# Kernel tuning notes

Measured on AMD Instinct MI355X. Metric: run time of the kernel, lower is better.

## Reference

```python
import jax, jax.numpy as jnp
import numpy as np

D_MODEL = 1024
NUM_HEADS = 16
HEAD_DIM = D_MODEL // NUM_HEADS
SCALE = HEAD_DIM ** -0.5
LN_EPS = 1e-5
Q_EPS = 1e-5


def bit_quant(W):
    # BitNet b1.58 ternary weight quantization with straight-through estimator.
    gamma = jnp.mean(jnp.abs(W))
    Wq = jnp.clip(jnp.round(W / (gamma + Q_EPS)), -1.0, 1.0) * gamma
    return W + jax.lax.stop_gradient(Wq - W)


def layer_norm(x, gamma, beta):
    mu = jnp.mean(x, axis=-1, keepdims=True)
    var = jnp.mean(jnp.square(x - mu), axis=-1, keepdims=True)
    return (x - mu) * jax.lax.rsqrt(var + LN_EPS) * gamma + beta


def setup_inputs() -> dict:
    key = jax.random.key(0)
    ks = jax.random.split(key, 8)
    B, T, T_ctx, C = 4, 1024, 2048, D_MODEL
    w_std = C ** -0.5
    return {
        "x": jax.random.normal(ks[0], (B, T, C), jnp.float32),
        "context": jax.random.normal(ks[1], (B, T_ctx, C), jnp.float32),
        "Wq": jax.random.normal(ks[2], (C, C), jnp.float32) * w_std,
        "bq": jnp.zeros((C,), jnp.float32),
        "Wk": jax.random.normal(ks[3], (C, C), jnp.float32) * w_std,
        "bk": jnp.zeros((C,), jnp.float32),
        "Wv": jax.random.normal(ks[4], (C, C), jnp.float32) * w_std,
        "bv": jnp.zeros((C,), jnp.float32),
        "Wo": jax.random.normal(ks[5], (C, C), jnp.float32) * w_std,
        "bo": jnp.zeros((C,), jnp.float32),
        "ln_gamma": jnp.ones((C,), jnp.float32),
        "ln_beta": jnp.zeros((C,), jnp.float32),
    }


def reference(x, context, Wq, bq, Wk, bk, Wv, bv, Wo, bo, ln_gamma, ln_beta):
    B, T, C = x.shape
    T_ctx = context.shape[1]
    residual = x
    xn = layer_norm(x, ln_gamma, ln_beta)
    # BitNet-quantized projections (torch Linear: y = x @ W.T + b)
    q = xn @ bit_quant(Wq).T + bq                      # [B,T,C]
    k = context @ bit_quant(Wk).T + bk                 # [B,T_ctx,C]
    v = context @ bit_quant(Wv).T + bv                 # [B,T_ctx,C]
    q = q.reshape(B, T, NUM_HEADS, HEAD_DIM)
    k = k.reshape(B, T_ctx, NUM_HEADS, HEAD_DIM)
    v = v.reshape(B, T_ctx, NUM_HEADS, HEAD_DIM)
    scores = jnp.einsum("bqhd,bkhd->bhqk", q, k) * SCALE   # [B,H,T,T_ctx]
    probs = jax.nn.softmax(scores, axis=-1)
    out = jnp.einsum("bhqk,bkhd->bqhd", probs, v).reshape(B, T, C)
    return residual + (out @ bit_quant(Wo).T + bo)
```

## Files before the change

kernel.cpp:

```cpp
#include <hip/hip_runtime.h>
#include <hip/hip_bf16.h>

typedef __attribute__((ext_vector_type(8))) short s8x;
typedef __attribute__((ext_vector_type(4))) float f4x;
typedef unsigned short u16;
typedef unsigned int u32;

#define T_ 1024
#define TC_ 2048
#define SCLOG2E 0.1803368801111243f

#define WAIT_VM(n) asm volatile("s_waitcnt vmcnt(" #n ")" ::: "memory")

__device__ __forceinline__ u16 f2bf(float f) {
    u32 u = __float_as_uint(f);
    return (u16)((u + 0x7fffu + ((u >> 16) & 1u)) >> 16);
}

#if defined(__has_builtin)
#if __has_builtin(__builtin_amdgcn_cvt_pk_bf16_f32)
#define HAVE_PK 1
#endif
#endif

__device__ __forceinline__ u32 pack2bf(float a, float b) {
#ifdef HAVE_PK
    typedef __attribute__((ext_vector_type(2))) __bf16 bf2t;
    bf2t r = __builtin_amdgcn_cvt_pk_bf16_f32(a, b);
    u32 u;
    __builtin_memcpy(&u, &r, 4);
    return u;
#else
    return (u32)f2bf(a) | ((u32)f2bf(b) << 16);
#endif
}

__device__ __forceinline__ void gload16(const void* g, void* l) {
    __builtin_amdgcn_global_load_lds((const __attribute__((address_space(1))) u32*)g,
                                     (__attribute__((address_space(3))) u32*)l, 16, 0, 0);
}

__global__ __launch_bounds__(256) void absmean_k(const float* __restrict__ W0, const float* __restrict__ W1,
                                                 const float* __restrict__ W2, const float* __restrict__ W3,
                                                 float* __restrict__ gsum) {
    int wi = blockIdx.y;
    const float* W = (wi == 0) ? W0 : (wi == 1) ? W1 : (wi == 2) ? W2 : W3;
    const int n4 = (1024 * 1024) / 4;
    float s = 0.f;
    int stride = gridDim.x * blockDim.x;
    for (int i = blockIdx.x * blockDim.x + threadIdx.x; i < n4; i += stride) {
        float4 v = ((const float4*)W)[i];
        s += fabsf(v.x) + fabsf(v.y) + fabsf(v.z) + fabsf(v.w);
    }
#pragma unroll
    for (int off = 32; off; off >>= 1) s += __shfl_down(s, off, 64);
    __shared__ float ps[4];
    if ((threadIdx.x & 63) == 0) ps[threadIdx.x >> 6] = s;
    __syncthreads();
    if (threadIdx.x == 0) atomicAdd(gsum + wi, ps[0] + ps[1] + ps[2] + ps[3]);
}

__global__ __launch_bounds__(256) void prep_k(
        const float* __restrict__ x, const float* __restrict__ lng, const float* __restrict__ lnb,
        u16* __restrict__ xn,
        const float* __restrict__ ctx, u16* __restrict__ ctxb,
        const float* __restrict__ W0, const float* __restrict__ W1,
        const float* __restrict__ W2, const float* __restrict__ W3,
        u16* __restrict__ D0, u16* __restrict__ D1, u16* __restrict__ D2, u16* __restrict__ D3,
        const float* __restrict__ gsum) {
    __shared__ float ps[8];
    int bx = blockIdx.x, t = threadIdx.x;
    if (bx < 4096) {
        int row = bx;
        float4 xv = ((const float4*)(x + (long)row * 1024))[t];
        float s = xv.x + xv.y + xv.z + xv.w;
        float s2 = xv.x * xv.x + xv.y * xv.y + xv.z * xv.z + xv.w * xv.w;
#pragma unroll
        for (int off = 32; off; off >>= 1) { s += __shfl_down(s, off, 64); s2 += __shfl_down(s2, off, 64); }
        if ((t & 63) == 0) { ps[t >> 6] = s; ps[4 + (t >> 6)] = s2; }
        __syncthreads();
        float S = ps[0] + ps[1] + ps[2] + ps[3];
        float S2 = ps[4] + ps[5] + ps[6] + ps[7];
        float mu = S * (1.f / 1024.f);
        float var = S2 * (1.f / 1024.f) - mu * mu;
        float rstd = rsqrtf(var + 1e-5f);
        float4 gv = ((const float4*)lng)[t];
        float4 bv = ((const float4*)lnb)[t];
        uint2 o;
        o.x = pack2bf((xv.x - mu) * rstd * gv.x + bv.x, (xv.y - mu) * rstd * gv.y + bv.y);
        o.y = pack2bf((xv.z - mu) * rstd * gv.z + bv.z, (xv.w - mu) * rstd * gv.w + bv.w);
        ((uint2*)(xn + (long)row * 1024))[t] = o;
    } else if (bx < 12288) {
        int i = (bx - 4096) * 256 + t;
        float4 v = ((const float4*)ctx)[i];
        uint2 o = {pack2bf(v.x, v.y), pack2bf(v.z, v.w)};
        ((uint2*)ctxb)[i] = o;
    } else {
        int wi = (bx - 12288) >> 10;
        const float* W = (wi == 0) ? W0 : (wi == 1) ? W1 : (wi == 2) ? W2 : W3;
        u16* D = (wi == 0) ? D0 : (wi == 1) ? D1 : (wi == 2) ? D2 : D3;
        float inv = 1.0f / (gsum[wi] * (1.0f / 1048576.0f) + 1e-5f);
        int i = ((bx - 12288) & 1023) * 256 + t;
        float4 wv = ((const float4*)W)[i];
        uint2 o;
        o.x = pack2bf(fminf(1.f, fmaxf(-1.f, rintf(wv.x * inv))),
                      fminf(1.f, fmaxf(-1.f, rintf(wv.y * inv))));
        o.y = pack2bf(fminf(1.f, fmaxf(-1.f, rintf(wv.z * inv))),
                      fminf(1.f, fmaxf(-1.f, rintf(wv.w * inv))));
        ((uint2*)D)[i] = o;
    }
}

__global__ __launch_bounds__(256) void gemm_fused(
        const u16* __restrict__ xn, const u16* __restrict__ ctxb,
        const u16* __restrict__ wtq, const u16* __restrict__ wtk, const u16* __restrict__ wtv,
        const float* __restrict__ bq, const float* __restrict__ bk, const float* __restrict__ bv,
        const float* __restrict__ gsum,
        u16* __restrict__ qb, u16* __restrict__ kb, u16* __restrict__ vtb) {
    __shared__ __align__(16) char smem[49152];
    int tid = threadIdx.x;
    int w = tid >> 6, l = tid & 63, lq = l & 15, lh = l >> 4;
    int wm = (w >> 1) * 64, wn = (w & 1) * 64;
    int bx = blockIdx.x;
    int xcd = bx & 7;
    int prob, m0, n0, gidx;
    const u16 *A, *Wt;
    const float* bias;
    float sc;
    if (bx < 256) {
        int local = bx >> 3;
        prob = 0; A = xn; Wt = wtq; bias = bq; sc = SCLOG2E; gidx = 0;
        m0 = (xcd * 4 + (local & 3)) * 128;
        n0 = (local >> 2) * 128;
    } else {
        int b = bx - 256;
        int local3 = b >> 3;
        int kv = local3 & 1;
        int idx = local3 >> 1;
        prob = 1 + kv; A = ctxb;
        Wt = kv ? wtv : wtk; bias = kv ? bv : bk; sc = 1.0f; gidx = 1 + kv;
        m0 = (xcd * 8 + (idx & 7)) * 128;
        n0 = (idx >> 3) * 128;
    }
    int sp = tid >> 3, ss = tid & 7;
    int st = ss ^ (sp & 7);
    int r0 = sp * 2 + (st >> 2), c0 = st & 3;
    const u16* Ag0 = A + (long)(m0 + r0) * 1024 + c0 * 8;
    const u16* Ag1 = Ag0 + 64 * 1024;
    const u16* Bg0 = Wt + (long)(n0 + r0) * 1024 + c0 * 8;
    const u16* Bg1 = Bg0 + 64 * 1024;
    int aoff[4], boff[4];
#pragma unroll
    for (int i = 0; i < 4; i++) {
        int ar = wm + i * 16 + lq, ap = ar >> 1;
        aoff[i] = ap * 128 + (((((ar & 1) << 2) | lh) ^ (ap & 7)) * 16);
        int br = wn + i * 16 + lq, bp = br >> 1;
        boff[i] = bp * 128 + (((((br & 1) << 2) | lh) ^ (bp & 7)) * 16);
    }
    f4x acc[4][4] = {};
#define STAGE_G(kt, buf)                                                   \
    {                                                                      \
        char* Ad = smem + (buf) * 16384;                                   \
        char* Bd = Ad + 8192;                                              \
        gload16(Ag0 + (kt) * 32, Ad + tid * 16);                           \
        gload16(Ag1 + (kt) * 32, Ad + 4096 + tid * 16);                    \
        gload16(Bg0 + (kt) * 32, Bd + tid * 16);                           \
        gload16(Bg1 + (kt) * 32, Bd + 4096 + tid * 16);                    \
    }
    STAGE_G(0, 0);
    STAGE_G(1, 1);
#pragma unroll
    for (int kt = 0; kt < 32; kt++) {
        if (kt < 31) { WAIT_VM(4); } else { WAIT_VM(0); }
        __builtin_amdgcn_s_barrier();
        if (kt + 2 < 32) STAGE_G(kt + 2, (kt + 2) % 3);
        const char* Ac = smem + (kt % 3) * 16384;
        const char* Bc = Ac + 8192;
        s8x af[4], bfr[4];
#pragma unroll
        for (int i = 0; i < 4; i++) {
            af[i] = *(const s8x*)(Ac + aoff[i]);
            bfr[i] = *(const s8x*)(Bc + boff[i]);
        }
#pragma unroll
        for (int i = 0; i < 4; i++)
#pragma unroll
            for (int j = 0; j < 4; j++)
                acc[i][j] = __builtin_amdgcn_mfma_f32_16x16x32_bf16(af[i], bfr[j], acc[i][j], 0, 0, 0);
    }
    float gamma = gsum[gidx] * (1.0f / 1048576.0f) * sc;
    if (prob < 2) {
        u16* outq = (prob == 0) ? qb : kb;
        int tshift = (prob == 0) ? 10 : 11;
        int tmask = (1 << tshift) - 1;
#pragma unroll
        for (int i = 0; i < 4; i++) {
            int gr = m0 + wm + i * 16 + lh * 4;
#pragma unroll
            for (int j = 0; j < 4; j++) {
                int gc = n0 + wn + j * 16 + lq;
                float bb = bias[gc] * sc;
                int h = gc >> 6, d = gc & 63;
#pragma unroll
                for (int r = 0; r < 4; r++) {
                    int row = gr + r;
                    int bidx = row >> tshift, tt = row & tmask;
                    outq[((((long)(bidx * 16 + h)) << tshift) + tt) * 64 + d] = f2bf(acc[i][j][r] * gamma + bb);
                }
            }
        }
    } else {
        __syncthreads();
        char* Ct = smem;
#pragma unroll
        for (int i = 0; i < 4; i++) {
            int tt = wm + i * 16 + lh * 4;
#pragma unroll
            for (int j = 0; j < 4; j++) {
                int c = wn + j * 16 + lq;
                float bb = bias[n0 + c];
                uint2 pk;
                pk.x = pack2bf(acc[i][j][0] * gamma + bb, acc[i][j][1] * gamma + bb);
                pk.y = pack2bf(acc[i][j][2] * gamma + bb, acc[i][j][3] * gamma + bb);
                int slot = (tt >> 3) ^ (c & 15);
                *(uint2*)(Ct + c * 256 + slot * 16 + (tt & 7) * 2) = pk;
            }
        }
        __syncthreads();
        int bb2 = m0 >> 11, t0 = m0 & 2047;
#pragma unroll
        for (int it = 0; it < 8; it++) {
            int e = it * 256 + tid;
            int c = e >> 4, ch = e & 15;
            int slot = ch ^ (c & 15);
            s8x v = *(const s8x*)(Ct + c * 256 + slot * 16);
            int gcg = n0 + c;
            int h = gcg >> 6, d = gcg & 63;
            *(s8x*)(vtb + ((long)((bb2 * 16 + h) * 64 + d)) * TC_ + t0 + ch * 8) = v;
        }
    }
}

__global__ __launch_bounds__(256) void gemm_o(const u16* __restrict__ A, const u16* __restrict__ Wt,
                                              const float* __restrict__ bias, const float* __restrict__ gsum,
                                              const float* __restrict__ residual, float* __restrict__ outr) {
    __shared__ __align__(16) char smem[36864];
    int tid = threadIdx.x;
    int w = tid >> 6, l = tid & 63, lq = l & 15, lh = l >> 4;
    int wm = (w >> 1) * 64, wn = (w & 1) * 32;
    int bx = blockIdx.x;
    int xcd = bx & 7, local = bx >> 3;
    int m0 = (xcd * 4 + (local & 3)) * 128;
    int n0 = (local >> 2) * 64;
    int sp = tid >> 3, ss = tid & 7;
    int st = ss ^ (sp & 7);
    int r0 = sp * 2 + (st >> 2), c0 = st & 3;
    const u16* Ag0 = A + (long)(m0 + r0) * 1024 + c0 * 8;
    const u16* Ag1 = Ag0 + 64 * 1024;
    const u16* Bg0 = Wt + (long)(n0 + r0) * 1024 + c0 * 8;
    int aoff[4], boff[2];
#pragma unroll
    for (int i = 0; i < 4; i++) {
        int ar = wm + i * 16 + lq, ap = ar >> 1;
        aoff[i] = ap * 128 + (((((ar & 1) << 2) | lh) ^ (ap & 7)) * 16);
    }
#pragma unroll
    for (int j = 0; j < 2; j++) {
        int br = wn + j * 16 + lq, bp = br >> 1;
        boff[j] = bp * 128 + (((((br & 1) << 2) | lh) ^ (bp & 7)) * 16);
    }
    f4x acc[4][2] = {};
#define STAGE_O(kt, buf)                                                   \
    {                                                                      \
        char* Ad = smem + (buf) * 12288;                                   \
        char* Bd = Ad + 8192;                                              \
        gload16(Ag0 + (kt) * 32, Ad + tid * 16);                           \
        gload16(Ag1 + (kt) * 32, Ad + 4096 + tid * 16);                    \
        gload16(Bg0 + (kt) * 32, Bd + tid * 16);                           \
    }
    STAGE_O(0, 0);
    STAGE_O(1, 1);
#pragma unroll
    for (int kt = 0; kt < 32; kt++) {
        if (kt < 31) { WAIT_VM(3); } else { WAIT_VM(0); }
        __builtin_amdgcn_s_barrier();
        if (kt + 2 < 32) STAGE_O(kt + 2, (kt + 2) % 3);
        const char* Ac = smem + (kt % 3) * 12288;
        const char* Bc = Ac + 8192;
        s8x af[4], bfr[2];
#pragma unroll
        for (int i = 0; i < 4; i++) af[i] = *(const s8x*)(Ac + aoff[i]);
#pragma unroll
        for (int j = 0; j < 2; j++) bfr[j] = *(const s8x*)(Bc + boff[j]);
#pragma unroll
        for (int i = 0; i < 4; i++)
#pragma unroll
            for (int j = 0; j < 2; j++)
                acc[i][j] = __builtin_amdgcn_mfma_f32_16x16x32_bf16(af[i], bfr[j], acc[i][j], 0, 0, 0);
    }
    float gamma = gsum[3] * (1.0f / 1048576.0f);
#pragma unroll
    for (int i = 0; i < 4; i++) {
        int gr = m0 + wm + i * 16 + lh * 4;
#pragma unroll
        for (int j = 0; j < 2; j++) {
            int gc = n0 + wn + j * 16 + lq;
            float bb = bias[gc];
#pragma unroll
            for (int r = 0; r < 4; r++) {
                long idx = (long)(gr + r) * 1024 + gc;
                outr[idx] = residual[idx] + acc[i][j][r] * gamma + bb;
            }
        }
    }
}

__global__ __launch_bounds__(256) void attn_k(const u16* __restrict__ qh, const u16* __restrict__ kh,
                                              const u16* __restrict__ vth, u16* __restrict__ attn) {
    __shared__ __align__(16) char smem[51200];
    int tid = threadIdx.x, w = tid >> 6, l = tid & 63, lq = l & 15, lh = l >> 4;
    int bh = blockIdx.x, q0 = blockIdx.y * 128;
    const u16* qp = qh + ((long)bh * T_ + q0) * 64;
    const u16* kp = kh + (long)bh * TC_ * 64;
    const u16* vp = vth + (long)bh * 64 * TC_;
#pragma unroll
    for (int i = 0; i < 4; i++) {
        int cid = i * 256 + tid;
        int r = cid >> 3, c = (cid & 7) ^ (r & 7);
        gload16(qp + r * 64 + c * 8, smem + cid * 16);
    }
    __syncthreads();
    s8x qf[2][2];
#pragma unroll
    for (int nb = 0; nb < 2; nb++)
#pragma unroll
        for (int dh = 0; dh < 2; dh++) {
            int qrow = w * 32 + nb * 16 + lq;
            int ch = (dh * 4 + lh) ^ (qrow & 7);
            qf[nb][dh] = *(const s8x*)(smem + qrow * 128 + ch * 16);
        }
    __syncthreads();
#define STAGE_KV(kt, buf)                                                          \
    {                                                                              \
        char* Kb = smem + (buf) * 16384;                                           \
        char* Vb = Kb + 8192;                                                      \
        _Pragma("unroll") for (int i = 0; i < 2; i++) {                            \
            int cid = i * 256 + tid;                                               \
            int r = cid >> 3, c = (cid & 7) ^ (r & 7);                             \
            gload16(kp + ((kt) * 64 + r) * 64 + c * 8, Kb + cid * 16);             \
            gload16(vp + (long)r * TC_ + (kt) * 64 + c * 8, Vb + cid * 16);        \
        }                                                                          \
    }
    STAGE_KV(0, 0);
    f4x oacc[2][4] = {};
    f4x lrun[2] = {};
    const s8x ones = {16256, 16256, 16256, 16256, 16256, 16256, 16256, 16256};
    char* Psb = smem + 32768 + w * 4608;
    for (int kt = 0; kt < TC_ / 64; kt++) {
        __syncthreads();
        if (kt + 1 < TC_ / 64) STAGE_KV(kt + 1, (kt + 1) & 1);
        char* Ksb = smem + (kt & 1) * 16384;
        char* Vsb = Ksb + 8192;
        f4x z[2][4];
#pragma unroll
        for (int ni = 0; ni < 4; ni++) {
            int kr = ni * 16 + lq;
            s8x a0 = *(const s8x*)(Ksb + kr * 128 + ((lh) ^ (kr & 7)) * 16);
            s8x a1 = *(const s8x*)(Ksb + kr * 128 + ((4 + lh) ^ (kr & 7)) * 16);
#pragma unroll
            for (int nb = 0; nb < 2; nb++) {
                f4x zz = {0.f, 0.f, 0.f, 0.f};
                zz = __builtin_amdgcn_mfma_f32_16x16x32_bf16(a0, qf[nb][0], zz, 0, 0, 0);
                zz = __builtin_amdgcn_mfma_f32_16x16x32_bf16(a1, qf[nb][1], zz, 0, 0, 0);
                z[nb][ni] = zz;
            }
        }
#pragma unroll
        for (int nb = 0; nb < 2; nb++) {
            int prow = nb * 16 + lq;
#pragma unroll
            for (int ni = 0; ni < 4; ni++) {
                uint2 pk;
                pk.x = pack2bf(__builtin_amdgcn_exp2f(z[nb][ni][0]), __builtin_amdgcn_exp2f(z[nb][ni][1]));
                pk.y = pack2bf(__builtin_amdgcn_exp2f(z[nb][ni][2]), __builtin_amdgcn_exp2f(z[nb][ni][3]));
                *(uint2*)(Psb + prow * 144 + ni * 32 + lh * 8) = pk;
            }
        }
        s8x vf[4][2];
#pragma unroll
        for (int nd = 0; nd < 4; nd++) {
            int vr = nd * 16 + lq;
            vf[nd][0] = *(const s8x*)(Vsb + vr * 128 + ((lh) ^ (vr & 7)) * 16);
            vf[nd][1] = *(const s8x*)(Vsb + vr * 128 + ((4 + lh) ^ (vr & 7)) * 16);
        }
#pragma unroll
        for (int qb = 0; qb < 2; qb++) {
            int prow = qb * 16 + lq;
            s8x pf0 = *(const s8x*)(Psb + prow * 144 + lh * 16);
            s8x pf1 = *(const s8x*)(Psb + prow * 144 + 64 + lh * 16);
            f4x rs = {0.f, 0.f, 0.f, 0.f};
            rs = __builtin_amdgcn_mfma_f32_16x16x32_bf16(pf0, ones, rs, 0, 0, 0);
            rs = __builtin_amdgcn_mfma_f32_16x16x32_bf16(pf1, ones, rs, 0, 0, 0);
#pragma unroll
            for (int r = 0; r < 4; r++) lrun[qb][r] += rs[r];
#pragma unroll
            for (int nd = 0; nd < 4; nd++) {
                oacc[qb][nd] = __builtin_amdgcn_mfma_f32_16x16x32_bf16(pf0, vf[nd][0], oacc[qb][nd], 0, 0, 0);
                oacc[qb][nd] = __builtin_amdgcn_mfma_f32_16x16x32_bf16(pf1, vf[nd][1], oacc[qb][nd], 0, 0, 0);
            }
        }
    }
    int b = bh >> 4, h = bh & 15;
#pragma unroll
    for (int qb = 0; qb < 2; qb++)
#pragma unroll
        for (int r = 0; r < 4; r++) {
            int q = q0 + w * 32 + qb * 16 + lh * 4 + r;
            float rcp = 1.f / lrun[qb][r];
#pragma unroll
            for (int nd = 0; nd < 4; nd++)
                attn[((long)(b * T_ + q)) * 1024 + h * 64 + nd * 16 + lq] = f2bf(oacc[qb][nd][r] * rcp);
        }
}

extern "C" void kernel_launch(void* const* d_in, const int* in_sizes, int n_in,
                              void* d_out, int out_size, void* d_ws, size_t ws_size,
                              hipStream_t stream) {
    const float* x   = (const float*)d_in[0];
    const float* ctx = (const float*)d_in[1];
    const float* Wq  = (const float*)d_in[2];
    const float* bq  = (const float*)d_in[3];
    const float* Wk  = (const float*)d_in[4];
    const float* bk  = (const float*)d_in[5];
    const float* Wv  = (const float*)d_in[6];
    const float* bv  = (const float*)d_in[7];
    const float* Wo  = (const float*)d_in[8];
    const float* bo  = (const float*)d_in[9];
    const float* lng = (const float*)d_in[10];
    const float* lnb = (const float*)d_in[11];
    float* out = (float*)d_out;

    char* ws = (char*)d_ws;
    float* gsum = (float*)ws;
    size_t off = 256;
    u16* wtq  = (u16*)(ws + off); off += (size_t)1024 * 1024 * 2;
    u16* wtk  = (u16*)(ws + off); off += (size_t)1024 * 1024 * 2;
    u16* wtv  = (u16*)(ws + off); off += (size_t)1024 * 1024 * 2;
    u16* wto  = (u16*)(ws + off); off += (size_t)1024 * 1024 * 2;
    u16* ctxb = (u16*)(ws + off); off += (size_t)8192 * 1024 * 2;
    u16* xn   = (u16*)(ws + off); off += (size_t)4096 * 1024 * 2;
    u16* qb_  = (u16*)(ws + off); off += (size_t)4096 * 1024 * 2;
    u16* kb   = (u16*)(ws + off); off += (size_t)8192 * 1024 * 2;
    u16* vtb  = (u16*)(ws + off); off += (size_t)8192 * 1024 * 2;
    u16* attnb = xn;

    hipMemsetAsync(gsum, 0, 16, stream);
    absmean_k<<<dim3(128, 4), 256, 0, stream>>>(Wq, Wk, Wv, Wo, gsum);
    prep_k<<<16384, 256, 0, stream>>>(x, lng, lnb, xn, ctx, ctxb,
                                      Wq, Wk, Wv, Wo, wtq, wtk, wtv, wto, gsum);
    gemm_fused<<<1280, 256, 0, stream>>>(xn, ctxb, wtq, wtk, wtv, bq, bk, bv, gsum, qb_, kb, vtb);
    attn_k<<<dim3(64, 8), 256, 0, stream>>>(qb_, kb, vtb, attnb);
    gemm_o<<<512, 256, 0, stream>>>(attnb, wto, bo, gsum, x, out);
}
```

Baseline: 254.1 us.

## Keep attention probabilities in registers and triple-buffer K/V loads

The attention kernel now computes S^T tiles and feeds the exponentiated probabilities directly from registers into 16x16x16 bf16 MFMAs that produce the transposed output. This removes the LDS round-trip for P and the extra ones-MFMA used for row sums, which are now accumulated in VALU and reduced with cross-lane shuffles at the end. K/V staging moves from double to triple buffering with explicit vmcnt waits and raw barriers, and the loop is fully unrolled. In exchange it uses more MFMA instructions of a smaller shape and puts more pressure on registers and on the unrolled code size.

```diff
diff --git a/kernel.cpp b/kernel.cpp
--- a/kernel.cpp
+++ b/kernel.cpp
@@ -2,6 +2,7 @@
 #include <hip/hip_bf16.h>
 
 typedef __attribute__((ext_vector_type(8))) short s8x;
+typedef __attribute__((ext_vector_type(4))) short s4x;
 typedef __attribute__((ext_vector_type(4))) float f4x;
 typedef unsigned short u16;
 typedef unsigned int u32;
@@ -20,6 +21,9 @@
 #if defined(__has_builtin)
 #if __has_builtin(__builtin_amdgcn_cvt_pk_bf16_f32)
 #define HAVE_PK 1
+#endif
+#if __has_builtin(__builtin_amdgcn_mfma_f32_16x16x16bf16_1k)
+#define HAVE_MFMA16 1
 #endif
 #endif
 
@@ -32,6 +36,16 @@
     return u;
 #else
     return (u32)f2bf(a) | ((u32)f2bf(b) << 16);
+#endif
+}
+
+__device__ __forceinline__ f4x mfma16(s4x a, s4x b, f4x c) {
+#ifdef HAVE_MFMA16
+    return __builtin_amdgcn_mfma_f32_16x16x16bf16_1k(a, b, c, 0, 0, 0);
+#else
+    f4x d = c;
+    asm volatile("v_mfma_f32_16x16x16_bf16 %0, %1, %2, %0" : "+v"(d) : "v"(a), "v"(b));
+    return d;
 #endif
 }
 
@@ -317,7 +331,7 @@
 
 __global__ __launch_bounds__(256) void attn_k(const u16* __restrict__ qh, const u16* __restrict__ kh,
                                               const u16* __restrict__ vth, u16* __restrict__ attn) {
-    __shared__ __align__(16) char smem[51200];
+    __shared__ __align__(16) char smem[49152];
     int tid = threadIdx.x, w = tid >> 6, l = tid & 63, lq = l & 15, lh = l >> 4;
     int bh = blockIdx.x, q0 = blockIdx.y * 128;
     const u16* qp = qh + ((long)bh * T_ + q0) * 64;
@@ -327,7 +341,7 @@
     for (int i = 0; i < 4; i++) {
         int cid = i * 256 + tid;
         int r = cid >> 3, c = (cid & 7) ^ (r & 7);
-        gload16(qp + r * 64 + c * 8, smem + cid * 16);
+        gload16(qp + r * 64 + c * 8, smem + 32768 + cid * 16);
     }
     __syncthreads();
     s8x qf[2][2];
@@ -337,90 +351,91 @@
         for (int dh = 0; dh < 2; dh++) {
             int qrow = w * 32 + nb * 16 + lq;
             int ch = (dh * 4 + lh) ^ (qrow & 7);
-            qf[nb][dh] = *(const s8x*)(smem + qrow * 128 + ch * 16);
+            qf[nb][dh] = *(const s8x*)(smem + 32768 + qrow * 128 + ch * 16);
         }
     __syncthreads();
 #define STAGE_KV(kt, buf)                                                          \
     {                                                                              \
         char* Kb = smem + (buf) * 16384;                                           \
         char* Vb = Kb + 8192;                                                      \
-        _Pragma("unroll") for (int i = 0; i < 2; i++) {                            \
-            int cid = i * 256 + tid;                                               \
-            int r = cid >> 3, c = (cid & 7) ^ (r & 7);                             \
-            gload16(kp + ((kt) * 64 + r) * 64 + c * 8, Kb + cid * 16);             \
-            gload16(vp + (long)r * TC_ + (kt) * 64 + c * 8, Vb + cid * 16);        \
-        }                                                                          \
+        int r = tid >> 3, c = (tid & 7) ^ (r & 7);                                 \
+        gload16(kp + ((kt) * 64 + r) * 64 + c * 8, Kb + tid * 16);                 \
+        gload16(kp + ((kt) * 64 + r + 32) * 64 + c * 8, Kb + 4096 + tid * 16);     \
+        gload16(vp + (long)r * TC_ + (kt) * 64 + c * 8, Vb + tid * 16);            \
+        gload16(vp + (long)(r + 32) * TC_ + (kt) * 64 + c * 8, Vb + 4096 + tid * 16); \
     }
     STAGE_KV(0, 0);
-    f4x oacc[2][4] = {};
-    f4x lrun[2] = {};
-    const s8x ones = {16256, 16256, 16256, 16256, 16256, 16256, 16256, 16256};
-    char* Psb = smem + 32768 + w * 4608;
-    for (int kt = 0; kt < TC_ / 64; kt++) {
-        __syncthreads();
-        if (kt + 1 < TC_ / 64) STAGE_KV(kt + 1, (kt + 1) & 1);
-        char* Ksb = smem + (kt & 1) * 16384;
-        char* Vsb = Ksb + 8192;
-        f4x z[2][4];
+    STAGE_KV(1, 1);
+    f4x oaccT[2][4] = {};
+    float lsum[2] = {};
+    int voff[4][4];
+#pragma unroll
+    for (int nd = 0; nd < 4; nd++)
 #pragma unroll
         for (int ni = 0; ni < 4; ni++) {
-            int kr = ni * 16 + lq;
-            s8x a0 = *(const s8x*)(Ksb + kr * 128 + ((lh) ^ (kr & 7)) * 16);
-            s8x a1 = *(const s8x*)(Ksb + kr * 128 + ((4 + lh) ^ (kr & 7)) * 16);
+            int vr = nd * 16 + lq;
+            voff[nd][ni] = vr * 128 + (((ni * 2 + (lh >> 1)) ^ (vr & 7)) * 16) + (lh & 1) * 8;
+        }
+    int koff[4][2];
+#pragma unroll
+    for (int ni = 0; ni < 4; ni++) {
+        int kr = ni * 16 + lq;
+        koff[ni][0] = kr * 128 + ((lh ^ (kr & 7)) * 16);
+        koff[ni][1] = kr * 128 + (((4 + lh) ^ (kr & 7)) * 16);
+    }
+#pragma unroll
+    for (int kt = 0; kt < 32; kt++) {
+        if (kt < 31) { WAIT_VM(4); } else { WAIT_VM(0); }
+        __builtin_amdgcn_s_barrier();
+        if (kt + 2 < 32) STAGE_KV(kt + 2, (kt + 2) % 3);
+        const char* Ksb = smem + (kt % 3) * 16384;
+        const char* Vsb = Ksb + 8192;
+#pragma unroll
+        for (int ni = 0; ni < 4; ni++) {
+            s8x a0 = *(const s8x*)(Ksb + koff[ni][0]);
+            s8x a1 = *(const s8x*)(Ksb + koff[ni][1]);
+            s4x pf[2];
 #pragma unroll
             for (int nb = 0; nb < 2; nb++) {
                 f4x zz = {0.f, 0.f, 0.f, 0.f};
                 zz = __builtin_amdgcn_mfma_f32_16x16x32_bf16(a0, qf[nb][0], zz, 0, 0, 0);
                 zz = __builtin_amdgcn_mfma_f32_16x16x32_bf16(a1, qf[nb][1], zz, 0, 0, 0);
-                z[nb][ni] = zz;
+                float e0 = __builtin_amdgcn_exp2f(zz[0]);
+                float e1 = __builtin_amdgcn_exp2f(zz[1]);
+                float e2 = __builtin_amdgcn_exp2f(zz[2]);
+                float e3 = __builtin_amdgcn_exp2f(zz[3]);
+                lsum[nb] += (e0 + e1) + (e2 + e3);
+                u32 p01 = pack2bf(e0, e1), p23 = pack2bf(e2, e3);
+                s4x pv;
+                __builtin_memcpy(&pv, &p01, 4);
+                __builtin_memcpy(((char*)&pv) + 4, &p23, 4);
+                pf[nb] = pv;
             }
-        }
-#pragma unroll
-        for (int nb = 0; nb < 2; nb++) {
-            int prow = nb * 16 + lq;
-#pragma unroll
-            for (int ni = 0; ni < 4; ni++) {
-                uint2 pk;
-                pk.x = pack2bf(__builtin_amdgcn_exp2f(z[nb][ni][0]), __builtin_amdgcn_exp2f(z[nb][ni][1]));
-                pk.y = pack2bf(__builtin_amdgcn_exp2f(z[nb][ni][2]), __builtin_amdgcn_exp2f(z[nb][ni][3]));
-                *(uint2*)(Psb + prow * 144 + ni * 32 + lh * 8) = pk;
+#pragma unroll
+            for (int nd = 0; nd < 4; nd++) {
+                s4x vf = *(const s4x*)(Vsb + voff[nd][ni]);
+                oaccT[0][nd] = mfma16(vf, pf[0], oaccT[0][nd]);
+                oaccT[1][nd] = mfma16(vf, pf[1], oaccT[1][nd]);
             }
         }
-        s8x vf[4][2];
+    }
+    int b = bh >> 4, h = bh & 15;
+#pragma unroll
+    for (int nb = 0; nb < 2; nb++) {
+        float s = lsum[nb];
+        s += __shfl_xor(s, 16, 64);
+        s += __shfl_xor(s, 32, 64);
+        float rcp = 1.f / s;
+        int q = q0 + w * 32 + nb * 16 + lq;
+        u16* dst = attn + ((long)(b * T_ + q)) * 1024 + h * 64 + lh * 4;
 #pragma unroll
         for (int nd = 0; nd < 4; nd++) {
-            int vr = nd * 16 + lq;
-            vf[nd][0] = *(const s8x*)(Vsb + vr * 128 + ((lh) ^ (vr & 7)) * 16);
-            vf[nd][1] = *(const s8x*)(Vsb + vr * 128 + ((4 + lh) ^ (vr & 7)) * 16);
-        }
-#pragma unroll
-        for (int qb = 0; qb < 2; qb++) {
-            int prow = qb * 16 + lq;
-            s8x pf0 = *(const s8x*)(Psb + prow * 144 + lh * 16);
-            s8x pf1 = *(const s8x*)(Psb + prow * 144 + 64 + lh * 16);
-            f4x rs = {0.f, 0.f, 0.f, 0.f};
-            rs = __builtin_amdgcn_mfma_f32_16x16x32_bf16(pf0, ones, rs, 0, 0, 0);
-            rs = __builtin_amdgcn_mfma_f32_16x16x32_bf16(pf1, ones, rs, 0, 0, 0);
-#pragma unroll
-            for (int r = 0; r < 4; r++) lrun[qb][r] += rs[r];
-#pragma unroll
-            for (int nd = 0; nd < 4; nd++) {
-                oacc[qb][nd] = __builtin_amdgcn_mfma_f32_16x16x32_bf16(pf0, vf[nd][0], oacc[qb][nd], 0, 0, 0);
-                oacc[qb][nd] = __builtin_amdgcn_mfma_f32_16x16x32_bf16(pf1, vf[nd][1], oacc[qb][nd], 0, 0, 0);
-            }
-        }
-    }
-    int b = bh >> 4, h = bh & 15;
-#pragma unroll
-    for (int qb = 0; qb < 2; qb++)
-#pragma unroll
-        for (int r = 0; r < 4; r++) {
-            int q = q0 + w * 32 + qb * 16 + lh * 4 + r;
-            float rcp = 1.f / lrun[qb][r];
-#pragma unroll
-            for (int nd = 0; nd < 4; nd++)
-                attn[((long)(b * T_ + q)) * 1024 + h * 64 + nd * 16 + lq] = f2bf(oacc[qb][nd][r] * rcp);
-        }
+            uint2 o;
+            o.x = pack2bf(oaccT[nb][nd][0] * rcp, oaccT[nb][nd][1] * rcp);
+            o.y = pack2bf(oaccT[nb][nd][2] * rcp, oaccT[nb][nd][3] * rcp);
+            *(uint2*)(dst + nd * 16) = o;
+        }
+    }
 }
 
 extern "C" void kernel_launch(void* const* d_in, const int* in_sizes, int n_in,
```

After: 427.6 us. +68.2%, slower.
